# Kernel tuning notes

Measured on AMD Instinct MI355X. Metric: run time of the kernel, lower is better.

The kernel has to match this reference:

```python
import jax, jax.numpy as jnp
import numpy as np

# Module hyperparameters (from init_kwargs)
H, W = 256, 256
NUM_ANGLE, NUM_RHO = 360, 360
MASK_WIDTH = 3.0
N, C = 16, 1


def setup_inputs() -> dict:
    key = jax.random.key(0)
    hough_map = jax.random.uniform(key, (N, C, NUM_ANGLE, NUM_RHO), dtype=jnp.float32)
    return {"hough_map": hough_map}


def _peak_mask(hough_map):
    # max_pool2d(k=3, s=1, p=1) local-max detection + 0.5*global-max threshold
    pooled = jax.lax.reduce_window(
        hough_map, -jnp.inf, jax.lax.max,
        window_dimensions=(1, 1, 3, 3), window_strides=(1, 1, 1, 1), padding="SAME")
    gmax = jnp.max(hough_map, axis=(-2, -1), keepdims=True)
    return (hough_map == pooled) & (hough_map > 0.5 * gmax)


def reference(hough_map):
    n, c, A, R = hough_map.shape
    peak = _peak_mask(hough_map).astype(jnp.float32)  # [N,C,A,R], 0/1

    # xy grid centered at image center (matches torch meshgrid indexing='ij')
    yv = jnp.arange(H, dtype=jnp.float32) - (H - 1) / 2
    xv = jnp.arange(W, dtype=jnp.float32) - (W - 1) / 2
    yy, xx = jnp.meshgrid(yv, xv, indexing="ij")
    xflat, yflat = xx.ravel(), yy.ravel()  # [H*W]

    delta_rho = 2.0 * float(np.sqrt((W / 2) ** 2 + (H / 2) ** 2)) / (NUM_RHO - 1)
    rho_vals = (jnp.arange(R, dtype=jnp.float32) - R / 2) * delta_rho  # [R]
    thetas = jnp.arange(A, dtype=jnp.float32) * (np.pi / NUM_ANGLE)    # [A]
    cos_t, sin_t = jnp.cos(thetas), jnp.sin(thetas)

    # Per (n,c): out = any over peaks (a,r) of |cos_a*x + sin_a*y - rho_r| < w.
    # Since peak/line masks are 0/1, max-over-peaks == (boolean matmul > 0).
    # Scan over angles to avoid materializing the [A,R,H*W] line tensor.
    peak_per_a = peak.reshape(n * c, A, R).transpose(1, 0, 2)  # [A, NC, R]

    def body(carry, inp):
        ct, st, pk = inp                       # pk: [NC, R]
        rho_cal = ct * xflat + st * yflat      # [HW]
        line = (jnp.abs(rho_cal[None, :] - rho_vals[:, None]) < MASK_WIDTH)
        hit = pk @ line.astype(jnp.float32)    # [NC, HW]
        return jnp.maximum(carry, jnp.where(hit > 0, 1.0, 0.0)), None

    init = jnp.zeros((n * c, H * W), jnp.float32)
    out, _ = jax.lax.scan(body, init, (cos_t, sin_t, peak_per_a))
    return out.reshape(n, c, H, W)
```

## Files before the change

kernel.cpp:

```cpp
#include <hip/hip_runtime.h>
#include <math.h>

#define NN 16
#define AA 360
#define RR 360
#define HH 256
#define WW 256
#define WORDS 7
#define BPI 32
#define BAND 8
#define NBAND (AA / BAND)

__global__ void k_gmax_tables(const float* __restrict__ h, float* __restrict__ part,
                              float* __restrict__ tab, float dtheta) {
    const int b = blockIdx.x;
    const int t = threadIdx.x;
    if (b < NN * BPI) {
        const int n  = b / BPI;
        const int bi = b % BPI;
        const float4* p = (const float4*)(h + (size_t)n * (AA * RR));
        const int n4 = (AA * RR) / 4;
        float m = 0.0f;
        for (int i = bi * 256 + t; i < n4; i += BPI * 256) {
            const float4 v = p[i];
            m = fmaxf(m, fmaxf(fmaxf(v.x, v.y), fmaxf(v.z, v.w)));
        }
        #pragma unroll
        for (int s = 32; s > 0; s >>= 1) m = fmaxf(m, __shfl_down(m, s, 64));
        __shared__ float red[4];
        if ((t & 63) == 0) red[t >> 6] = m;
        __syncthreads();
        if (t == 0) part[n * BPI + bi] = fmaxf(fmaxf(red[0], red[1]), fmaxf(red[2], red[3]));
    } else {
        for (int a = t; a < AA; a += 256) {
            float th = __fmul_rn((float)a, dtheta);
            tab[a]      = (float)cos((double)th);
            tab[AA + a] = (float)sin((double)th);
        }
    }
}

__global__ void k_peaks(const float* __restrict__ h, const float* __restrict__ part,
                        unsigned long long* __restrict__ bits) {
    __shared__ float rows[BAND + 2][RR];
    __shared__ float gth;
    const int n    = blockIdx.x / NBAND;
    const int band = blockIdx.x % NBAND;
    const int a0   = band * BAND;
    const int t    = threadIdx.x;

    if (t < 64) {
        float m = (t < BPI) ? part[n * BPI + t] : 0.0f;
        #pragma unroll
        for (int s = 32; s > 0; s >>= 1) m = fmaxf(m, __shfl_down(m, s, 64));
        if (t == 0) gth = 0.5f * m;
    }

    if (a0 > 0 && a0 + BAND < AA) {
        const float4* src = (const float4*)(h + ((size_t)n * AA + a0 - 1) * RR);
        float4* dst = (float4*)&rows[0][0];
        for (int i = t; i < (BAND + 2) * RR / 4; i += 384) dst[i] = src[i];
    } else {
        for (int i = t; i < (BAND + 2) * RR; i += 384) {
            const int aa = a0 - 1 + i / RR;
            ((float*)rows)[i] = (aa >= 0 && aa < AA)
                ? h[((size_t)n * AA + aa) * RR + (i - (i / RR) * RR)] : -INFINITY;
        }
    }
    __syncthreads();

    const int r = t;
    const float th = gth;
    #pragma unroll
    for (int k = 0; k < BAND; ++k) {
        bool pk = false;
        if (r < RR) {
            const float v = rows[k + 1][r];
            if (v > th) {
                pk = true;
                #pragma unroll
                for (int j = 0; j < 3; ++j) {
                    #pragma unroll
                    for (int dr = -1; dr <= 1; ++dr) {
                        if (j == 1 && dr == 0) continue;
                        const int rr = r + dr;
                        if (rr < 0 || rr >= RR) continue;
                        if (rows[k + j][rr] > v) pk = false;
                    }
                }
            }
        }
        const unsigned long long m = __ballot(pk);
        if ((t & 63) == 0)
            bits[((size_t)n * AA + a0 + k) * WORDS + (t >> 6)] = m;
    }
    if (t < BAND)
        bits[((size_t)n * AA + a0 + t) * WORDS + 6] = 0ull;
}

__device__ __forceinline__ bool fhit(float rc, int r, float drho) {
    const float rho = __fmul_rn((float)(r - 180), drho);
    return fabsf(__fsub_rn(rc, rho)) < 3.0f;
}

__global__ void __launch_bounds__(256)
k_out(const unsigned long long* __restrict__ bits,
      const float* __restrict__ tab,
      float* __restrict__ out, float inv_dr, float drho) {
    __shared__ __align__(16) unsigned long long Lb[AA * WORDS];
    __shared__ float Lct[AA], Lst[AA];
    const int n     = blockIdx.x >> 7;
    const int chunk = blockIdx.x & 127;
    const int t     = threadIdx.x;

    {
        const uint4* src = (const uint4*)(bits + (size_t)n * AA * WORDS);
        uint4* dst = (uint4*)Lb;
        for (int i = t; i < AA * WORDS / 2; i += 256) dst[i] = src[i];
        for (int i = t; i < AA; i += 256) {
            Lct[i] = tab[i];
            Lst[i] = tab[AA + i];
        }
    }
    __syncthreads();

    const int pbase = chunk * 512 + t;
    #pragma unroll
    for (int q = 0; q < 2; ++q) {
        const int p = pbase + q * 256;
        const int y = p >> 8;
        const int x = p & 255;
        const float xf = (float)x - 127.5f;
        const float yf = (float)y - 127.5f;
        float res = 0.0f;
        for (int a = 0; a < AA; ++a) {
            const float rc = __fadd_rn(__fmul_rn(Lct[a], xf), __fmul_rn(Lst[a], yf));
            const int lo_est = (int)ceilf (__fmul_rn(__fsub_rn(rc, 3.0f), inv_dr)) + 180;
            const int hi_est = (int)floorf(__fmul_rn(__fadd_rn(rc, 3.0f), inv_dr)) + 180;
            int lo = fhit(rc, lo_est - 1, drho) ? lo_est - 1
                   : (fhit(rc, lo_est, drho) ? lo_est : lo_est + 1);
            int hi = fhit(rc, hi_est + 1, drho) ? hi_est + 1
                   : (fhit(rc, hi_est, drho) ? hi_est : hi_est - 1);
            lo = lo < 0 ? 0 : lo;
            hi = hi > RR - 1 ? RR - 1 : hi;
            if (lo <= hi) {
                const int len = hi - lo + 1;
                const unsigned long long part = (1ull << len) - 1ull;
                const int sh = lo & 63;
                const int w  = lo >> 6;
                const unsigned long long m0 = part << sh;
                const unsigned long long m1 = sh ? (part >> (64 - sh)) : 0ull;
                const unsigned long long v0 = Lb[a * WORDS + w];
                const unsigned long long v1 = Lb[a * WORDS + w + 1];
                if ((v0 & m0) | (v1 & m1)) { res = 1.0f; break; }
            }
        }
        out[(size_t)n * (HH * WW) + p] = res;
    }
}

extern "C" void kernel_launch(void* const* d_in, const int* in_sizes, int n_in,
                              void* d_out, int out_size, void* d_ws, size_t ws_size,
                              hipStream_t stream) {
    const float* h = (const float*)d_in[0];
    float* out = (float*)d_out;

    char* ws = (char*)d_ws;
    unsigned long long* bits = (unsigned long long*)ws;
    float* part = (float*)(ws + (size_t)NN * AA * WORDS * 8);
    float* tab  = part + NN * BPI;

    const double dr_d = 2.0 * sqrt((WW / 2.0) * (WW / 2.0) + (HH / 2.0) * (HH / 2.0)) / (RR - 1);
    const float drho   = (float)dr_d;
    const float inv_dr = (float)(1.0 / dr_d);
    const float dtheta = (float)(3.14159265358979323846 / 360.0);

    k_gmax_tables<<<NN * BPI + 1, 256, 0, stream>>>(h, part, tab, dtheta);
    k_peaks<<<NN * NBAND, 384, 0, stream>>>(h, part, bits);
    k_out<<<NN * 128, 256, 0, stream>>>(bits, tab, out, inv_dr, drho);
}
```

Before: 80.31 us.

## Fuse gmax, peak detection and line rendering into one cooperative kernel

```diff
diff --git a/kernel.cpp b/kernel.cpp
--- a/kernel.cpp
+++ b/kernel.cpp
@@ -1,4 +1,5 @@
 #include <hip/hip_runtime.h>
+#include <hip/hip_cooperative_groups.h>
 #include <math.h>
 
 #define NN 16
@@ -7,75 +8,89 @@
 #define HH 256
 #define WW 256
 #define WORDS 7
-#define BPI 32
 #define BAND 8
 #define NBAND (AA / BAND)
+#define NBLK (NN * NBAND)
+#define NTHR 384
+#define CHUNK 1457
 
-__global__ void k_gmax_tables(const float* __restrict__ h, float* __restrict__ part,
-                              float* __restrict__ tab, float dtheta) {
-    const int b = blockIdx.x;
-    const int t = threadIdx.x;
-    if (b < NN * BPI) {
-        const int n  = b / BPI;
-        const int bi = b % BPI;
-        const float4* p = (const float4*)(h + (size_t)n * (AA * RR));
-        const int n4 = (AA * RR) / 4;
-        float m = 0.0f;
-        for (int i = bi * 256 + t; i < n4; i += BPI * 256) {
-            const float4 v = p[i];
-            m = fmaxf(m, fmaxf(fmaxf(v.x, v.y), fmaxf(v.z, v.w)));
+namespace cg = cooperative_groups;
+
+__device__ __forceinline__ bool fhit(float rc, int r, float drho) {
+    const float rho = __fmul_rn((float)(r - 180), drho);
+    return fabsf(__fsub_rn(rc, rho)) < 3.0f;
+}
+
+__global__ void __launch_bounds__(NTHR)
+k_fused(const float* __restrict__ h, float* __restrict__ part, float* __restrict__ tab,
+        unsigned long long* __restrict__ bits, float* __restrict__ out,
+        float dtheta, float drho, float inv_dr) {
+    __shared__ __align__(16) union {
+        struct { float rows[BAND + 2][RR]; } ab;
+        struct { unsigned long long Lb[AA * WORDS];
+                 float ct[AA], st[AA]; } c;
+    } S;
+    __shared__ float s_red[6];
+    __shared__ float s_gth;
+
+    const int blk  = blockIdx.x;
+    const int n    = blk / NBAND;
+    const int band = blk % NBAND;
+    const int a0   = band * BAND;
+    const int t    = threadIdx.x;
+
+    if (a0 > 0 && a0 + BAND < AA) {
+        const float4* src = (const float4*)(h + ((size_t)n * AA + a0 - 1) * RR);
+        float4* dst = (float4*)&S.ab.rows[0][0];
+        for (int i = t; i < (BAND + 2) * RR / 4; i += NTHR) dst[i] = src[i];
+    } else {
+        for (int i = t; i < (BAND + 2) * RR; i += NTHR) {
+            const int aa = a0 - 1 + i / RR;
+            (&S.ab.rows[0][0])[i] = (aa >= 0 && aa < AA)
+                ? h[((size_t)n * AA + aa) * RR + (i - (i / RR) * RR)] : -INFINITY;
         }
-        #pragma unroll
-        for (int s = 32; s > 0; s >>= 1) m = fmaxf(m, __shfl_down(m, s, 64));
-        __shared__ float red[4];
-        if ((t & 63) == 0) red[t >> 6] = m;
-        __syncthreads();
-        if (t == 0) part[n * BPI + bi] = fmaxf(fmaxf(red[0], red[1]), fmaxf(red[2], red[3]));
-    } else {
-        for (int a = t; a < AA; a += 256) {
+    }
+    if (blk == 0) {
+        for (int a = t; a < AA; a += NTHR) {
             float th = __fmul_rn((float)a, dtheta);
             tab[a]      = (float)cos((double)th);
             tab[AA + a] = (float)sin((double)th);
         }
     }
-}
+    __syncthreads();
 
-__global__ void k_peaks(const float* __restrict__ h, const float* __restrict__ part,
-                        unsigned long long* __restrict__ bits) {
-    __shared__ float rows[BAND + 2][RR];
-    __shared__ float gth;
-    const int n    = blockIdx.x / NBAND;
-    const int band = blockIdx.x % NBAND;
-    const int a0   = band * BAND;
-    const int t    = threadIdx.x;
+    {
+        const float* cen = &S.ab.rows[1][0];
+        float m = 0.0f;
+        for (int i = t; i < BAND * RR; i += NTHR) m = fmaxf(m, cen[i]);
+        #pragma unroll
+        for (int s = 32; s > 0; s >>= 1) m = fmaxf(m, __shfl_down(m, s, 64));
+        if ((t & 63) == 0) s_red[t >> 6] = m;
+        __syncthreads();
+        if (t == 0) {
+            m = s_red[0];
+            #pragma unroll
+            for (int i = 1; i < 6; ++i) m = fmaxf(m, s_red[i]);
+            part[blk] = m;
+        }
+    }
+
+    cg::this_grid().sync();
 
     if (t < 64) {
-        float m = (t < BPI) ? part[n * BPI + t] : 0.0f;
+        float m = (t < NBAND) ? part[n * NBAND + t] : 0.0f;
         #pragma unroll
         for (int s = 32; s > 0; s >>= 1) m = fmaxf(m, __shfl_down(m, s, 64));
-        if (t == 0) gth = 0.5f * m;
-    }
-
-    if (a0 > 0 && a0 + BAND < AA) {
-        const float4* src = (const float4*)(h + ((size_t)n * AA + a0 - 1) * RR);
-        float4* dst = (float4*)&rows[0][0];
-        for (int i = t; i < (BAND + 2) * RR / 4; i += 384) dst[i] = src[i];
-    } else {
-        for (int i = t; i < (BAND + 2) * RR; i += 384) {
-            const int aa = a0 - 1 + i / RR;
-            ((float*)rows)[i] = (aa >= 0 && aa < AA)
-                ? h[((size_t)n * AA + aa) * RR + (i - (i / RR) * RR)] : -INFINITY;
-        }
+        if (t == 0) s_gth = 0.5f * m;
     }
     __syncthreads();
-
+    const float th = s_gth;
     const int r = t;
-    const float th = gth;
     #pragma unroll
     for (int k = 0; k < BAND; ++k) {
         bool pk = false;
         if (r < RR) {
-            const float v = rows[k + 1][r];
+            const float v = S.ab.rows[k + 1][r];
             if (v > th) {
                 pk = true;
                 #pragma unroll
@@ -85,7 +100,7 @@
                         if (j == 1 && dr == 0) continue;
                         const int rr = r + dr;
                         if (rr < 0 || rr >= RR) continue;
-                        if (rows[k + j][rr] > v) pk = false;
+                        if (S.ab.rows[k + j][rr] > v) pk = false;
                     }
                 }
             }
@@ -96,45 +111,30 @@
     }
     if (t < BAND)
         bits[((size_t)n * AA + a0 + t) * WORDS + 6] = 0ull;
-}
 
-__device__ __forceinline__ bool fhit(float rc, int r, float drho) {
-    const float rho = __fmul_rn((float)(r - 180), drho);
-    return fabsf(__fsub_rn(rc, rho)) < 3.0f;
-}
-
-__global__ void __launch_bounds__(256)
-k_out(const unsigned long long* __restrict__ bits,
-      const float* __restrict__ tab,
-      float* __restrict__ out, float inv_dr, float drho) {
-    __shared__ __align__(16) unsigned long long Lb[AA * WORDS];
-    __shared__ float Lct[AA], Lst[AA];
-    const int n     = blockIdx.x >> 7;
-    const int chunk = blockIdx.x & 127;
-    const int t     = threadIdx.x;
+    cg::this_grid().sync();
 
     {
         const uint4* src = (const uint4*)(bits + (size_t)n * AA * WORDS);
-        uint4* dst = (uint4*)Lb;
-        for (int i = t; i < AA * WORDS / 2; i += 256) dst[i] = src[i];
-        for (int i = t; i < AA; i += 256) {
-            Lct[i] = tab[i];
-            Lst[i] = tab[AA + i];
+        uint4* dst = (uint4*)S.c.Lb;
+        for (int i = t; i < AA * WORDS / 2; i += NTHR) dst[i] = src[i];
+        for (int i = t; i < AA; i += NTHR) {
+            S.c.ct[i] = tab[i];
+            S.c.st[i] = tab[AA + i];
         }
     }
     __syncthreads();
 
-    const int pbase = chunk * 512 + t;
-    #pragma unroll
-    for (int q = 0; q < 2; ++q) {
-        const int p = pbase + q * 256;
+    const int pbeg = band * CHUNK;
+    const int pend = (pbeg + CHUNK < HH * WW) ? pbeg + CHUNK : HH * WW;
+    for (int p = pbeg + t; p < pend; p += NTHR) {
         const int y = p >> 8;
         const int x = p & 255;
         const float xf = (float)x - 127.5f;
         const float yf = (float)y - 127.5f;
         float res = 0.0f;
         for (int a = 0; a < AA; ++a) {
-            const float rc = __fadd_rn(__fmul_rn(Lct[a], xf), __fmul_rn(Lst[a], yf));
+            const float rc = __fadd_rn(__fmul_rn(S.c.ct[a], xf), __fmul_rn(S.c.st[a], yf));
             const int lo_est = (int)ceilf (__fmul_rn(__fsub_rn(rc, 3.0f), inv_dr)) + 180;
             const int hi_est = (int)floorf(__fmul_rn(__fadd_rn(rc, 3.0f), inv_dr)) + 180;
             int lo = fhit(rc, lo_est - 1, drho) ? lo_est - 1
@@ -145,13 +145,13 @@
             hi = hi > RR - 1 ? RR - 1 : hi;
             if (lo <= hi) {
                 const int len = hi - lo + 1;
-                const unsigned long long part = (1ull << len) - 1ull;
+                const unsigned long long pmask = (1ull << len) - 1ull;
                 const int sh = lo & 63;
                 const int w  = lo >> 6;
-                const unsigned long long m0 = part << sh;
-                const unsigned long long m1 = sh ? (part >> (64 - sh)) : 0ull;
-                const unsigned long long v0 = Lb[a * WORDS + w];
-                const unsigned long long v1 = Lb[a * WORDS + w + 1];
+                const unsigned long long m0 = pmask << sh;
+                const unsigned long long m1 = sh ? (pmask >> (64 - sh)) : 0ull;
+                const unsigned long long v0 = S.c.Lb[a * WORDS + w];
+                const unsigned long long v1 = S.c.Lb[a * WORDS + w + 1];
                 if ((v0 & m0) | (v1 & m1)) { res = 1.0f; break; }
             }
         }
@@ -168,14 +168,14 @@
     char* ws = (char*)d_ws;
     unsigned long long* bits = (unsigned long long*)ws;
     float* part = (float*)(ws + (size_t)NN * AA * WORDS * 8);
-    float* tab  = part + NN * BPI;
+    float* tab  = part + NBLK;
 
     const double dr_d = 2.0 * sqrt((WW / 2.0) * (WW / 2.0) + (HH / 2.0) * (HH / 2.0)) / (RR - 1);
-    const float drho   = (float)dr_d;
-    const float inv_dr = (float)(1.0 / dr_d);
-    const float dtheta = (float)(3.14159265358979323846 / 360.0);
+    float drho   = (float)dr_d;
+    float inv_dr = (float)(1.0 / dr_d);
+    float dtheta = (float)(3.14159265358979323846 / 360.0);
 
-    k_gmax_tables<<<NN * BPI + 1, 256, 0, stream>>>(h, part, tab, dtheta);
-    k_peaks<<<NN * NBAND, 384, 0, stream>>>(h, part, bits);
-    k_out<<<NN * 128, 256, 0, stream>>>(bits, tab, out, inv_dr, drho);
+    void* args[] = { (void*)&h, (void*)&part, (void*)&tab, (void*)&bits,
+                     (void*)&out, (void*)&dtheta, (void*)&drho, (void*)&inv_dr };
+    hipLaunchCooperativeKernel((void*)k_fused, dim3(NBLK), dim3(NTHR), args, 0, stream);
 }
```

After: 213.4 us. 2.66x slower.
